# Kernel optimization log

Hardware: AMD Instinct MI355X
Metric: run time of the kernel (lower is better)

Reference implementation:

```python
import jax, jax.numpy as jnp
import numpy as np

B, T, M, C, H = 32, 128, 1290, 512, 8
NUM_BLOCKS = 4
MLP_LAYERS = 2
TOPK = 8


def _ln(x, g, b):
    mu = jnp.mean(x, -1, keepdims=True)
    var = jnp.mean((x - mu) ** 2, -1, keepdims=True)
    return (x - mu) / jnp.sqrt(var + 1e-5) * g + b


def setup_inputs() -> dict:
    key = jax.random.key(0)
    ks = jax.random.split(key, 12)

    def w(k, shape, s=0.02):
        return jax.random.normal(k, shape, jnp.float32) * s

    return {
        "ipts": jax.random.normal(ks[0], (B, T, C), jnp.float32),
        "memory": jax.random.normal(ks[1], (B, M, C), jnp.float32),
        "Wq": w(ks[2], (C, C)), "bq": jnp.zeros(C, jnp.float32),
        "Wk": w(ks[3], (C, C)), "bk": jnp.zeros(C, jnp.float32),
        "Wv": w(ks[4], (C, C)), "bv": jnp.zeros(C, jnp.float32),
        "Wm": w(ks[5], (C, C)), "bm": jnp.zeros(C, jnp.float32),  # shared attention_mlp layer
        "g1": jnp.ones(C, jnp.float32), "b1": jnp.zeros(C, jnp.float32),
        "g2": jnp.ones(C, jnp.float32), "b2": jnp.zeros(C, jnp.float32),
        "Wp": w(ks[6], (C, C)), "bp": jnp.zeros(C, jnp.float32),
        "rep_w": jax.random.normal(ks[7], (C,), jnp.float32),
        "Wig": w(ks[8], (C, 2 * C)), "big": jnp.zeros(2 * C, jnp.float32),
        "Wmg": w(ks[9], (C, 2 * C)), "bmg": jnp.zeros(2 * C, jnp.float32),
        "forget_bias": jnp.float32(1.0),
        "input_bias": jnp.float32(0.0),
    }


def reference(ipts, memory, Wq, bq, Wk, bk, Wv, bv, Wm, bm, g1, b1, g2, b2,
              Wp, bp, rep_w, Wig, big, Wmg, bmg, forget_bias, input_bias):
    Dh = C // H
    scale = 1.0 / np.sqrt(Dh)

    def heads(x):  # [B,L,C] -> [B,H,L,Dh]
        return x.reshape(x.shape[0], x.shape[1], H, Dh).transpose(0, 2, 1, 3)

    def mha(inp, mem, use_topk):
        # query from mem, key/value from inp (matches multi_head_attention(ipts, memory))
        q, k, v = heads(mem @ Wq + bq), heads(inp @ Wk + bk), heads(inp @ Wv + bv)
        att = jax.nn.softmax(jnp.einsum('bhqd,bhkd->bhqk', q, k) * scale, axis=-1)
        if use_topk:
            _, idx = jax.lax.top_k(att, TOPK)  # [B,H,Q,TOPK]
            mask = jnp.zeros_like(att)
            for i in range(TOPK):  # small fixed loop; avoids [.,.,.,K,L] blowup
                mask = mask + jax.nn.one_hot(idx[..., i], att.shape[-1], dtype=att.dtype)
            att = att * mask
        o = jnp.einsum('bhqk,bhkd->bhqd', att, v)
        return o.transpose(0, 2, 1, 3).reshape(o.shape[0], o.shape[2], C)

    inp = ipts @ Wp + bp  # input_projector, [B,T,C]
    mem = memory
    for _ in range(NUM_BLOCKS):
        mem = _ln(mem + mha(inp, mem, True), g1, b1)
        h = mem
        for _ in range(MLP_LAYERS):  # shared weights (ModuleList([lin]*L))
            h = jax.nn.relu(h @ Wm + bm)
        mem = _ln(mem + h, g2, b2)

    # gates (gate_style='unit')
    gi = jnp.mean(jax.nn.relu(rep_w * inp), axis=1) @ Wig + big  # [B,2C]
    gm = jnp.tanh(memory) @ Wmg + bmg                            # [B,M,2C]
    gates = gm + gi[:, None, :]
    ig = jax.nn.sigmoid(gates[..., :C] + input_bias)
    fg = jax.nn.sigmoid(gates[..., C:] + forget_bias)
    next_memory = ig * jnp.tanh(mem) + fg * memory

    # hx: query from inp, key/value from next_memory, no topk
    hx = mha(next_memory, inp, False)  # [B,T,C]
    return (next_memory, hx)
```

## Files before the change

### kernel.cpp

```cpp
#include <hip/hip_runtime.h>
#include <stdint.h>

typedef uint16_t u16;
typedef uint32_t u32;

#define DEVI __device__ __forceinline__

DEVI float b2f(u16 u) { return __uint_as_float(((u32)u) << 16); }
DEVI float blo(u32 u) { return __uint_as_float(u << 16); }
DEVI float bhi(u32 u) { return __uint_as_float(u & 0xffff0000u); }
DEVI u16 f2b(float f) {
  u32 x = __float_as_uint(f);
  return (u16)((x + 0x7fffu + ((x >> 16) & 1u)) >> 16);
}
DEVI u32 pack2(float a, float b) { return (u32)f2b(a) | ((u32)f2b(b) << 16); }
DEVI float sigm(float x) { return 1.f / (1.f + __expf(-x)); }

typedef __bf16 bf16x8 __attribute__((ext_vector_type(8)));
typedef float f32x4 __attribute__((ext_vector_type(4)));

#define MFMA16(a, b, c) __builtin_amdgcn_mfma_f32_16x16x32_bf16(a, b, c, 0, 0, 0)

DEVI void gll16(const void* g, void* l) {
  __builtin_amdgcn_global_load_lds((const __attribute__((address_space(1))) void*)g,
                                   (__attribute__((address_space(3))) void*)l, 16, 0, 0);
}

DEVI u32 fmono(float s) {
  u32 x = __float_as_uint(s);
  return x ^ (((u32)((int)x >> 31)) | 0x80000000u);
}

DEVI void ced(u32& a, u32& b) {
  u32 hi = max(a, b), lo = min(a, b);
  a = hi; b = lo;
}
DEVI void sort8_desc(u32* v) {
  ced(v[0], v[1]); ced(v[2], v[3]); ced(v[4], v[5]); ced(v[6], v[7]);
  ced(v[0], v[2]); ced(v[1], v[3]); ced(v[4], v[6]); ced(v[5], v[7]);
  ced(v[1], v[2]); ced(v[5], v[6]);
  ced(v[0], v[4]); ced(v[1], v[5]); ced(v[2], v[6]); ced(v[3], v[7]);
  ced(v[2], v[4]); ced(v[3], v[5]);
  ced(v[1], v[2]); ced(v[3], v[4]); ced(v[5], v[6]);
}
DEVI void bitonic8_desc(u32* v) {
  ced(v[0], v[4]); ced(v[1], v[5]); ced(v[2], v[6]); ced(v[3], v[7]);
  ced(v[0], v[2]); ced(v[1], v[3]); ced(v[4], v[6]); ced(v[5], v[7]);
  ced(v[0], v[1]); ced(v[2], v[3]); ced(v[4], v[5]); ced(v[6], v[7]);
}
DEVI void merge_top8(u32* a, const u32* b) {
#pragma unroll
  for (int j = 0; j < 8; ++j) a[j] = max(a[j], b[7 - j]);
  bitonic8_desc(a);
}

__global__ void detect_kernel(const u16* __restrict__ x, int* __restrict__ flag) {
  if (threadIdx.x == 0 && blockIdx.x == 0) {
    int f = 0;
    for (int i = 0; i < 64; ++i) {
      u16 u = x[2 * i];
      int e = (u >> 7) & 0xFF;
      if (e > 131) f = 1;
    }
    *flag = f;
  }
}

struct CvtArgs {
  const void* src[23];
  int aoff[23];
  int n[23];
  int total;
};

__global__ __launch_bounds__(256) void convert_fused(CvtArgs a, u16* __restrict__ arena,
                                                     const int* __restrict__ flag) {
  int e4 = (blockIdx.x * 256 + threadIdx.x) * 4;
  if (e4 >= a.total) return;
  const char* sp = (const char*)a.src[0];
  int rel = e4, cnt = a.n[0];
#pragma unroll
  for (int j = 1; j < 23; ++j)
    if (e4 >= a.aoff[j]) { sp = (const char*)a.src[j]; rel = e4 - a.aoff[j]; cnt = a.n[j]; }
  const bool f32 = (*flag != 0);
  if (rel + 3 < cnt) {
    if (f32) {
      float4 v = *(const float4*)(sp + (size_t)rel * 4);
      uint2 o;
      o.x = pack2(v.x, v.y);
      o.y = pack2(v.z, v.w);
      *(uint2*)(arena + e4) = o;
    } else {
      *(uint2*)(arena + e4) = *(const uint2*)(sp + (size_t)rel * 2);
    }
  } else {
#pragma unroll
    for (int k = 0; k < 4; ++k) {
      u16 o = 0;
      if (rel + k < cnt)
        o = f32 ? f2b(((const float*)sp)[rel + k]) : ((const u16*)sp)[rel + k];
      arena[e4 + k] = o;
    }
  }
}

__global__ void biascat_kernel(const u16* __restrict__ bq, const u16* __restrict__ bk,
                               const u16* __restrict__ bv, u16* __restrict__ bqkv,
                               u16* __restrict__ bkv) {
  int t = threadIdx.x;
  bqkv[t] = bq[t];
  bqkv[512 + t] = bk[t];
  bqkv[1024 + t] = bv[t];
  bkv[t] = bk[t];
  bkv[512 + t] = bv[t];
}

template <int ACT>
__global__ __launch_bounds__(256, 3) void gemm_bt(
    const u16* __restrict__ A, const u16* __restrict__ Bt,
    const u16* __restrict__ bias, u16* __restrict__ Co, int Mtot, int Ntot) {
  __shared__ __align__(16) u16 aT[128 * 64];
  __shared__ __align__(16) u16 bT[128 * 64];
  const int tid = threadIdx.x;
  const int lane = tid & 63;
  const int w = tid >> 6;
  const int m0 = blockIdx.x * 128;
  const int n0 = blockIdx.y * 128;
  const int wm = (w & 1) << 6;
  const int wn = (w >> 1) << 6;

  f32x4 acc[4][4] = {};

  const u16* ga[4];
  const u16* gb[4];
#pragma unroll
  for (int q = 0; q < 4; ++q) {
    int j = q * 256 + tid;
    int r = j >> 3, s = j & 7;
    int c = (s ^ (r & 7)) * 8;
    int ra = m0 + r;
    if (ra >= Mtot) ra = Mtot - 1;
    ga[q] = A + (size_t)ra * 512 + c;
    gb[q] = Bt + (size_t)(n0 + r) * 512 + c;
  }

  for (int ko = 0; ko < 8; ++ko) {
    const int k0 = ko * 64;
#pragma unroll
    for (int q = 0; q < 4; ++q) {
      int j = q * 256 + tid;
      gll16(ga[q] + k0, aT + j * 8);
      gll16(gb[q] + k0, bT + j * 8);
    }
    __syncthreads();
#pragma unroll
    for (int ks = 0; ks < 2; ++ks) {
      bf16x8 af[4], bfr[4];
#pragma unroll
      for (int i = 0; i < 4; ++i) {
        int cch = ks * 4 + (lane >> 4);
        int r = wm + i * 16 + (lane & 15);
        af[i] = *(const bf16x8*)(aT + (r * 8 + (cch ^ (r & 7))) * 8);
        int rn = wn + i * 16 + (lane & 15);
        bfr[i] = *(const bf16x8*)(bT + (rn * 8 + (cch ^ (rn & 7))) * 8);
      }
#pragma unroll
      for (int i = 0; i < 4; ++i)
#pragma unroll
        for (int jn = 0; jn < 4; ++jn)
          acc[i][jn] = MFMA16(af[i], bfr[jn], acc[i][jn]);
    }
    __syncthreads();
  }

  const int cl = lane & 15;
  const int rg = lane >> 4;
#pragma unroll
  for (int jn = 0; jn < 4; ++jn) {
    int col = n0 + wn + jn * 16 + cl;
    float bv = b2f(bias[col]);
#pragma unroll
    for (int i = 0; i < 4; ++i) {
      int rowb = m0 + wm + i * 16 + rg * 4;
#pragma unroll
      for (int rr = 0; rr < 4; ++rr) {
        int row = rowb + rr;
        if (row < Mtot) {
          float vv = acc[i][jn][rr] + bv;
          if (ACT) vv = fmaxf(vv, 0.f);
          Co[(size_t)row * Ntot + col] = f2b(vv);
        }
      }
    }
  }
}

__global__ __launch_bounds__(256) void transpose_kernel(const u16* __restrict__ in,
                                                        u16* __restrict__ outb, int K, int N) {
  __shared__ u16 tile[32][33];
  const int tx = threadIdx.x & 31, ty = threadIdx.x >> 5;
  const int bx = blockIdx.x * 32;
  const int by = blockIdx.y * 32;
#pragma unroll
  for (int i = 0; i < 32; i += 8) tile[ty + i][tx] = in[(size_t)(by + ty + i) * N + bx + tx];
  __syncthreads();
#pragma unroll
  for (int i = 0; i < 32; i += 8) outb[(size_t)(bx + ty + i) * K + by + tx] = tile[tx][ty + i];
}

__global__ void tanhmem_kernel(const u16* __restrict__ mi, u16* __restrict__ th, int n8) {
  int i = blockIdx.x * 256 + threadIdx.x;
  if (i >= n8) return;
  uint4 u = ((const uint4*)mi)[i];
  uint4 t;
  t.x = pack2(tanhf(blo(u.x)), tanhf(bhi(u.x)));
  t.y = pack2(tanhf(blo(u.y)), tanhf(bhi(u.y)));
  t.z = pack2(tanhf(blo(u.z)), tanhf(bhi(u.z)));
  t.w = pack2(tanhf(blo(u.w)), tanhf(bhi(u.w)));
  ((uint4*)th)[i] = t;
}

__global__ void redmean_kernel(const u16* __restrict__ inp, const u16* __restrict__ repw,
                               u16* __restrict__ outb) {
  const int b = blockIdx.x;
  const int c = blockIdx.y * 256 + threadIdx.x;
  const float rw = b2f(repw[c]);
  float s = 0.f;
  for (int t = 0; t < 128; ++t)
    s += fmaxf(rw * b2f(inp[(size_t)(b * 128 + t) * 512 + c]), 0.f);
  outb[b * 512 + c] = f2b(s * (1.f / 128.f));
}

__global__ __launch_bounds__(64) void ln_kernel(const u16* __restrict__ src,
                                                const u16* __restrict__ addb,
                                                u16* __restrict__ dst,
                                                const u16* __restrict__ g,
                                                const u16* __restrict__ bb) {
  const int row = blockIdx.x;
  const int lane = threadIdx.x;
  const u16* srow = src + (size_t)row * 512;
  const u16* arow = addb + (size_t)row * 512;
  float x[8];
  float s = 0.f;
#pragma unroll
  for (int i = 0; i < 8; ++i) {
    int c = lane + i * 64;
    x[i] = b2f(srow[c]) + b2f(arow[c]);
    s += x[i];
  }
#pragma unroll
  for (int off = 32; off > 0; off >>= 1) s += __shfl_xor(s, off, 64);
  const float mu = s * (1.f / 512.f);
  float v = 0.f;
#pragma unroll
  for (int i = 0; i < 8; ++i) {
    float d = x[i] - mu;
    v = fmaf(d, d, v);
  }
#pragma unroll
  for (int off = 32; off > 0; off >>= 1) v += __shfl_xor(v, off, 64);
  const float rstd = rsqrtf(v * (1.f / 512.f) + 1e-5f);
  u16* orow = dst + (size_t)row * 512;
#pragma unroll
  for (int i = 0; i < 8; ++i) {
    int c = lane + i * 64;
    orow[c] = f2b(fmaf((x[i] - mu) * rstd, b2f(g[c]), b2f(bb[c])));
  }
}

__global__ __launch_bounds__(256, 3) void attn1_mfma(const u16* __restrict__ q,
                                                     const u16* __restrict__ kb,
                                                     const u16* __restrict__ vb,
                                                     u16* __restrict__ o, int ldkv) {
  __shared__ __align__(16) u16 Pl[128 * 136];
  __shared__ __align__(16) u16 VT[64 * 136];
  __shared__ float lbuf[128];
  u16* Kl = Pl;

  const int tid = threadIdx.x;
  const int lane = tid & 63;
  const int w = tid >> 6;
  const int quad = lane >> 4;
  const int l15 = lane & 15;
  const int qb = blockIdx.x;
  const int bh = blockIdx.y;
  const int b = bh >> 3, h = bh & 7;

#pragma unroll
  for (int qq = 0; qq < 4; ++qq) {
    int j = qq * 256 + tid;
    int r = j >> 3, s = j & 7;
    gll16(kb + (size_t)(b * 128 + r) * ldkv + h * 64 + (s ^ (r & 7)) * 8, Kl + j * 8);
  }
#pragma unroll
  for (int p = 0; p < 4; ++p) {
    int key = (tid & 63) + 64 * (p & 1);
    int dc = w + 4 * (p >> 1);
    uint4 u = *(const uint4*)(vb + (size_t)(b * 128 + key) * ldkv + h * 64 + dc * 8);
    u16 tmp[8];
    *(uint4*)tmp = u;
#pragma unroll
    for (int jj = 0; jj < 8; ++jj) VT[(dc * 8 + jj) * 136 + key] = tmp[jj];
  }

  bf16x8 bq[2][2];
  {
    int ra = min(qb * 128 + w * 32 + l15, 1289);
    int rb_ = min(qb * 128 + w * 32 + 16 + l15, 1289);
    const u16* qa = q + (size_t)(b * 1290 + ra) * 512 + h * 64 + quad * 8;
    const u16* qc = q + (size_t)(b * 1290 + rb_) * 512 + h * 64 + quad * 8;
    bq[0][0] = *(const bf16x8*)(qa);
    bq[0][1] = *(const bf16x8*)(qa + 32);
    bq[1][0] = *(const bf16x8*)(qc);
    bq[1][1] = *(const bf16x8*)(qc + 32);
  }
  __syncthreads();

  f32x4 sa[2][8] = {};
#pragma unroll
  for (int ks = 0; ks < 2; ++ks) {
#pragma unroll
    for (int jn = 0; jn < 8; ++jn) {
      int n = jn * 16 + l15;
      int cch = ks * 4 + quad;
      bf16x8 ak = *(const bf16x8*)(Kl + (n * 8 + (cch ^ (n & 7))) * 8);
      sa[0][jn] = MFMA16(ak, bq[0][ks], sa[0][jn]);
      sa[1][jn] = MFMA16(ak, bq[1][ks], sa[1][jn]);
    }
  }
  __syncthreads();

  const u32 ibase = 127u - (u32)(quad * 4);
#pragma unroll
  for (int i = 0; i < 2; ++i) {
    const int qi = w * 32 + i * 16 + l15;
    u32 g[4][8];
#pragma unroll
    for (int jn = 0; jn < 8; ++jn)
#pragma unroll
      for (int rr = 0; rr < 4; ++rr) {
        float s = sa[i][jn][rr] * 0.125f;
        sa[i][jn][rr] = s;
        g[jn >> 1][(jn & 1) * 4 + rr] =
            (fmono(s) & 0xFFFFFF80u) | (ibase - (u32)(jn * 16 + rr));
      }
    sort8_desc(g[0]); sort8_desc(g[1]); sort8_desc(g[2]); sort8_desc(g[3]);
    merge_top8(g[0], g[1]);
    merge_top8(g[2], g[3]);
    merge_top8(g[0], g[2]);
    u32* tv = g[0];
#pragma unroll
    for (int off = 16; off < 64; off <<= 1) {
      u32 pv[8];
#pragma unroll
      for (int j = 0; j < 8; ++j) pv[j] = (u32)__shfl_xor((int)tv[7 - j], off, 64);
#pragma unroll
      for (int j = 0; j < 8; ++j) tv[j] = max(tv[j], pv[j]);
      bitonic8_desc(tv);
    }
    const u32 t8 = tv[7];
    u32 mb = tv[0] & 0xFFFFFF80u;
    u32 xm = (mb & 0x80000000u) ? (mb ^ 0x80000000u) : ~mb;
    const float mx = __uint_as_float(xm);
    float lsum = 0.f;
#pragma unroll
    for (int jn = 0; jn < 8; ++jn) {
      u16 pr[4];
#pragma unroll
      for (int rr = 0; rr < 4; ++rr) {
        float s = sa[i][jn][rr];
        float e = __expf(s - mx);
        lsum += e;
        u32 kk = (fmono(s) & 0xFFFFFF80u) | (ibase - (u32)(jn * 16 + rr));
        pr[rr] = (kk >= t8) ? f2b(e) : (u16)0;
      }
      uint2 st;
      st.x = (u32)pr[0] | ((u32)pr[1] << 16);
      st.y = (u32)pr[2] | ((u32)pr[3] << 16);
      *(uint2*)(Pl + qi * 136 + jn * 16 + quad * 4) = st;
    }
    lsum += __shfl_xor(lsum, 16, 64);
    lsum += __shfl_xor(lsum, 32, 64);
    if (quad == 0) lbuf[qi] = 1.f / lsum;
  }
  __syncthreads();

  f32x4 oa[2][4] = {};
#pragma unroll
  for (int kc = 0; kc < 4; ++kc) {
    bf16x8 ap[2];
#pragma unroll
    for (int i = 0; i < 2; ++i)
      ap[i] = *(const bf16x8*)(Pl + (w * 32 + i * 16 + l15) * 136 + kc * 32 + quad * 8);
#pragma unroll
    for (int jd = 0; jd < 4; ++jd) {
      bf16x8 bv_ = *(const bf16x8*)(VT + (jd * 16 + l15) * 136 + kc * 32 + quad * 8);
      oa[0][jd] = MFMA16(ap[0], bv_, oa[0][jd]);
      oa[1][jd] = MFMA16(ap[1], bv_, oa[1][jd]);
    }
  }

#pragma unroll
  for (int i = 0; i < 2; ++i) {
    int rowl = w * 32 + i * 16 + quad * 4;
#pragma unroll
    for (int rr = 0; rr < 4; ++rr) {
      int qg = qb * 128 + rowl + rr;
      if (qg < 1290) {
        float il = lbuf[rowl + rr];
        u16* orow = o + (size_t)(b * 1290 + qg) * 512 + h * 64;
#pragma unroll
        for (int jd = 0; jd < 4; ++jd) orow[jd * 16 + l15] = f2b(oa[i][jd][rr] * il);
      }
    }
  }
}

__global__ __launch_bounds__(256, 2) void attn2_mfma(const u16* __restrict__ q2,
                                                     const u16* __restrict__ k2,
                                                     const u16* __restrict__ v2,
                                                     float* __restrict__ pacc,
                                                     float* __restrict__ pml,
                                                     int ldq, int ldkv) {
  __shared__ __align__(16) u16 Kl[64 * 64];
  __shared__ __align__(16) u16 VT[64 * 72];
  __shared__ __align__(16) u16 Pl[4 * 32 * 72];
  const int tid = threadIdx.x;
  const int lane = tid & 63;
  const int w = tid >> 6;
  const int quad = lane >> 4;
  const int l15 = lane & 15;
  const int bh = blockIdx.x;
  const int b = bh >> 3, h = bh & 7;
  const int part = blockIdx.y;
  const int kstart = (part * 1290) >> 2;
  const int kend = ((part + 1) * 1290) >> 2;

  bf16x8 aq[2][2];
  {
    int r0 = b * 128 + w * 32 + l15;
    const u16* qa = q2 + (size_t)r0 * ldq + h * 64 + quad * 8;
    aq[0][0] = *(const bf16x8*)(qa);
    aq[0][1] = *(const bf16x8*)(qa + 32);
    aq[1][0] = *(const bf16x8*)(qa + (size_t)16 * ldq);
    aq[1][1] = *(const bf16x8*)(qa + (size_t)16 * ldq + 32);
  }

  f32x4 oa[2][4] = {};
  float m_[2][4], l_[2][4];
#pragma unroll
  for (int i = 0; i < 2; ++i)
#pragma unroll
    for (int r = 0; r < 4; ++r) { m_[i][r] = -1e30f; l_[i][r] = 0.f; }

  const int nk = kend - kstart;
  for (int kt = 0; kt < nk; kt += 64) {
    __syncthreads();
#pragma unroll
    for (int qq = 0; qq < 2; ++qq) {
      int j = qq * 256 + tid;
      int r = j >> 3, s = j & 7;
      int kg = kstart + kt + r;
      if (kg >= kend) kg = kend - 1;
      gll16(k2 + (size_t)(b * 1290 + kg) * ldkv + h * 64 + (s ^ (r & 7)) * 8, Kl + j * 8);
    }
    {
      int r = tid & 63;
      int kg = kstart + kt + r;
      if (kg >= kend) kg = kend - 1;
      const u16* vrow = v2 + (size_t)(b * 1290 + kg) * ldkv + h * 64;
#pragma unroll
      for (int p = 0; p < 2; ++p) {
        int dc = (tid >> 6) + p * 4;
        uint4 u = *(const uint4*)(vrow + dc * 8);
        u16 tmp[8];
        *(uint4*)tmp = u;
#pragma unroll
        for (int jj = 0; jj < 8; ++jj) VT[(dc * 8 + jj) * 72 + r] = tmp[jj];
      }
    }
    __syncthreads();

    f32x4 sa[2][4] = {};
#pragma unroll
    for (int ks = 0; ks < 2; ++ks) {
#pragma unroll
      for (int jn = 0; jn < 4; ++jn) {
        int n = jn * 16 + l15;
        int cch = ks * 4 + quad;
        bf16x8 bk = *(const bf16x8*)(Kl + (n * 8 + (cch ^ (n & 7))) * 8);
        sa[0][jn] = MFMA16(aq[0][ks], bk, sa[0][jn]);
        sa[1][jn] = MFMA16(aq[1][ks], bk, sa[1][jn]);
      }
    }

    u16* pw = Pl + w * (32 * 72);
#pragma unroll
    for (int i = 0; i < 2; ++i) {
      float rmax[4] = {-1e30f, -1e30f, -1e30f, -1e30f};
#pragma unroll
      for (int jn = 0; jn < 4; ++jn) {
        int kg = kstart + kt + jn * 16 + l15;
        bool val = kg < kend;
#pragma unroll
        for (int r = 0; r < 4; ++r) {
          float s = sa[i][jn][r] * 0.125f;
          s = val ? s : -1e30f;
          sa[i][jn][r] = s;
          rmax[r] = fmaxf(rmax[r], s);
        }
      }
#pragma unroll
      for (int off = 1; off < 16; off <<= 1)
#pragma unroll
        for (int r = 0; r < 4; ++r) rmax[r] = fmaxf(rmax[r], __shfl_xor(rmax[r], off, 64));
      float alpha[4];
#pragma unroll
      for (int r = 0; r < 4; ++r) {
        float mn = fmaxf(m_[i][r], rmax[r]);
        alpha[r] = __expf(m_[i][r] - mn);
        m_[i][r] = mn;
      }
      float lsum[4] = {0.f, 0.f, 0.f, 0.f};
#pragma unroll
      for (int jn = 0; jn < 4; ++jn)
#pragma unroll
        for (int r = 0; r < 4; ++r) {
          float p = __expf(sa[i][jn][r] - m_[i][r]);
          sa[i][jn][r] = p;
          lsum[r] += p;
        }
#pragma unroll
      for (int off = 1; off < 16; off <<= 1)
#pragma unroll
        for (int r = 0; r < 4; ++r) lsum[r] += __shfl_xor(lsum[r], off, 64);
#pragma unroll
      for (int r = 0; r < 4; ++r) l_[i][r] = l_[i][r] * alpha[r] + lsum[r];
#pragma unroll
      for (int jd = 0; jd < 4; ++jd)
#pragma unroll
        for (int r = 0; r < 4; ++r) oa[i][jd][r] *= alpha[r];
#pragma unroll
      for (int jn = 0; jn < 4; ++jn) {
        int col = jn * 16 + l15;
#pragma unroll
        for (int r = 0; r < 4; ++r)
          pw[(i * 16 + quad * 4 + r) * 72 + col] = f2b(sa[i][jn][r]);
      }
    }

#pragma unroll
    for (int ks = 0; ks < 2; ++ks) {
      bf16x8 ap[2];
#pragma unroll
      for (int i = 0; i < 2; ++i)
        ap[i] = *(const bf16x8*)(pw + (i * 16 + l15) * 72 + ks * 32 + quad * 8);
#pragma unroll
      for (int jd = 0; jd < 4; ++jd) {
        bf16x8 bv_ = *(const bf16x8*)(VT + (jd * 16 + l15) * 72 + ks * 32 + quad * 8);
        oa[0][jd] = MFMA16(ap[0], bv_, oa[0][jd]);
        oa[1][jd] = MFMA16(ap[1], bv_, oa[1][jd]);
      }
    }
  }

  float* pa = pacc + (size_t)(part * 256 + bh) * 128 * 64;
#pragma unroll
  for (int i = 0; i < 2; ++i) {
    int row = w * 32 + i * 16 + quad * 4;
#pragma unroll
    for (int r = 0; r < 4; ++r)
#pragma unroll
      for (int jd = 0; jd < 4; ++jd)
        pa[(size_t)(row + r) * 64 + jd * 16 + l15] = oa[i][jd][r];
    if (l15 == 0) {
#pragma unroll
      for (int r = 0; r < 4; ++r) {
        size_t pi = (size_t)(part * 256 + bh) * 128 + row + r;
        pml[pi * 2 + 0] = m_[i][r];
        pml[pi * 2 + 1] = l_[i][r];
      }
    }
  }
}

__global__ __launch_bounds__(64) void attn2_merge(const float* __restrict__ pacc,
                                                  const float* __restrict__ pml,
                                                  void* __restrict__ outp,
                                                  const int* __restrict__ flag) {
  const int qi = blockIdx.x;
  const int bh = qi >> 7, t = qi & 127;
  const int b = bh >> 3, h = bh & 7;
  const int lane = threadIdx.x;
  float mv[4], lv[4];
  float m0 = -1e30f;
#pragma unroll
  for (int i = 0; i < 4; ++i) {
    size_t pi = (size_t)(i * 256 + bh) * 128 + t;
    mv[i] = pml[pi * 2];
    lv[i] = pml[pi * 2 + 1];
    m0 = fmaxf(m0, mv[i]);
  }
  float L = 0.f, accd = 0.f;
#pragma unroll
  for (int i = 0; i < 4; ++i) {
    size_t pi = (size_t)(i * 256 + bh) * 128 + t;
    float e = __expf(mv[i] - m0);
    L += lv[i] * e;
    accd += pacc[pi * 64 + lane] * e;
  }
  float v = accd / L;
  size_t off = (size_t)41280 * 512 + ((size_t)(b * 128 + t) * 512 + h * 64 + lane);
  if (*flag) ((float*)outp)[off] = v; else ((u16*)outp)[off] = f2b(v);
}

__global__ __launch_bounds__(512) void gates_fused(const u16* __restrict__ gm,
                                                   const u16* __restrict__ gi,
                                                   const u16* __restrict__ memfin,
                                                   const u16* __restrict__ mem_in,
                                                   const u16* __restrict__ ibp,
                                                   const u16* __restrict__ fbp,
                                                   u16* __restrict__ nmbf,
                                                   void* __restrict__ outp,
                                                   const int* __restrict__ flag) {
  const int r = blockIdx.x;
  const int b = r / 1290;
  const int c = threadIdx.x;
  size_t i1024 = (size_t)r * 1024;
  size_t idx = (size_t)r * 512 + c;
  float ig = sigm(b2f(gm[i1024 + c]) + b2f(gi[b * 1024 + c]) + b2f(ibp[0]));
  float fg = sigm(b2f(gm[i1024 + 512 + c]) + b2f(gi[b * 1024 + 512 + c]) + b2f(fbp[0]));
  float v = ig * tanhf(b2f(memfin[idx])) + fg * b2f(mem_in[idx]);
  nmbf[idx] = f2b(v);
  if (*flag) ((float*)outp)[idx] = v; else ((u16*)outp)[idx] = f2b(v);
}

extern "C" void kernel_launch(void* const* d_in, const int* in_sizes, int n_in,
                              void* d_out, int out_size, void* d_ws, size_t ws_size,
                              hipStream_t stream) {
  (void)out_size; (void)ws_size;
  char* ws = (char*)d_ws;
  size_t off = 0;
  auto alloc = [&](size_t bytes) {
    char* p = ws + off;
    off += (bytes + 255) & ~(size_t)255;
    return (void*)p;
  };

  int* flag = (int*)alloc(256);

  size_t aoffs[32];
  size_t total = 0;
  for (int i = 0; i < n_in; ++i) {
    aoffs[i] = total;
    total += ((size_t)in_sizes[i] + 127) & ~(size_t)127;
  }
  u16* arena = (u16*)alloc(total * 2);

  const u16* c_ipts = arena + aoffs[0];
  const u16* c_mem  = arena + aoffs[1];
  const u16* c_Wq = arena + aoffs[2];  const u16* c_bq = arena + aoffs[3];
  const u16* c_Wk = arena + aoffs[4];  const u16* c_bk = arena + aoffs[5];
  const u16* c_Wv = arena + aoffs[6];  const u16* c_bv = arena + aoffs[7];
  const u16* c_Wm = arena + aoffs[8];  const u16* c_bm = arena + aoffs[9];
  const u16* c_g1 = arena + aoffs[10]; const u16* c_b1 = arena + aoffs[11];
  const u16* c_g2 = arena + aoffs[12]; const u16* c_b2 = arena + aoffs[13];
  const u16* c_Wp = arena + aoffs[14]; const u16* c_bp = arena + aoffs[15];
  const u16* c_repw = arena + aoffs[16];
  const u16* c_Wig = arena + aoffs[17]; const u16* c_big = arena + aoffs[18];
  const u16* c_Wmg = arena + aoffs[19]; const u16* c_bmg = arena + aoffs[20];
  const u16* c_fb = arena + aoffs[21];
  const u16* c_ib = arena + aoffs[22];

  u16* WqkvT = (u16*)alloc((size_t)1536 * 512 * 2);
  u16* WmT = (u16*)alloc(512 * 512 * 2);
  u16* WpT = (u16*)alloc(512 * 512 * 2);
  u16* WigT = (u16*)alloc(512 * 1024 * 2);
  u16* WmgT = (u16*)alloc(512 * 1024 * 2);
  u16* bqkv = (u16*)alloc(1536 * 2);
  u16* bkv = (u16*)alloc(1024 * 2);
  u16* inp = (u16*)alloc((size_t)4096 * 512 * 2);
  u16* qkvbuf = (u16*)alloc((size_t)4096 * 1536 * 2);
  u16* rmean = (u16*)alloc(32 * 512 * 2);
  u16* gi = (u16*)alloc(32 * 1024 * 2);
  u16* membf = (u16*)alloc((size_t)41280 * 512 * 2);
  u16* qbuf = (u16*)alloc((size_t)41280 * 512 * 2);
  u16* obuf = (u16*)alloc((size_t)41280 * 512 * 2);
  u16* gmbuf = (u16*)alloc((size_t)41280 * 512 * 2);
  u16* nmbf = (u16*)alloc((size_t)41280 * 512 * 2);
  (void)gmbuf;
  u16* gm1024 = obuf;
  u16* kvbuf = obuf;
  float* pacc = (float*)(void*)qbuf;
  float* pml = (float*)((char*)(void*)qbuf + (size_t)4 * 32768 * 64 * 4);

  detect_kernel<<<1, 64, 0, stream>>>((const u16*)d_in[0], flag);
  {
    CvtArgs ca;
    for (int i = 0; i < 23; ++i) {
      int ii = (i < n_in) ? i : (n_in - 1);
      ca.src[i] = d_in[ii];
      ca.aoff[i] = (int)aoffs[ii];
      ca.n[i] = in_sizes[ii];
    }
    ca.total = (int)total;
    convert_fused<<<(unsigned)((total / 4 + 255) / 256), 256, 0, stream>>>(ca, arena, flag);
  }
  biascat_kernel<<<1, 512, 0, stream>>>(c_bq, c_bk, c_bv, bqkv, bkv);

  transpose_kernel<<<dim3(16, 16), 256, 0, stream>>>(c_Wq, WqkvT, 512, 512);
  transpose_kernel<<<dim3(16, 16), 256, 0, stream>>>(c_Wk, WqkvT + (size_t)512 * 512, 512, 512);
  transpose_kernel<<<dim3(16, 16), 256, 0, stream>>>(c_Wv, WqkvT + (size_t)1024 * 512, 512, 512);
  transpose_kernel<<<dim3(16, 16), 256, 0, stream>>>(c_Wm, WmT, 512, 512);
  transpose_kernel<<<dim3(16, 16), 256, 0, stream>>>(c_Wp, WpT, 512, 512);
  transpose_kernel<<<dim3(32, 16), 256, 0, stream>>>(c_Wig, WigT, 512, 1024);
  transpose_kernel<<<dim3(32, 16), 256, 0, stream>>>(c_Wmg, WmgT, 512, 1024);

  gemm_bt<0><<<dim3(32, 4), 256, 0, stream>>>(c_ipts, WpT, c_bp, inp, 4096, 512);
  gemm_bt<0><<<dim3(32, 12), 256, 0, stream>>>(inp, WqkvT, bqkv, qkvbuf, 4096, 1536);

  redmean_kernel<<<dim3(32, 2), 256, 0, stream>>>(inp, c_repw, rmean);
  gemm_bt<0><<<dim3(1, 8), 256, 0, stream>>>(rmean, WigT, c_big, gi, 32, 1024);

  const u16* memsrc = c_mem;
  for (int it = 0; it < 4; ++it) {
    gemm_bt<0><<<dim3(323, 4), 256, 0, stream>>>(memsrc, WqkvT, c_bq, qbuf, 41280, 512);
    attn1_mfma<<<dim3(11, 256), 256, 0, stream>>>(qbuf, qkvbuf + 512, qkvbuf + 1024, obuf, 1536);
    ln_kernel<<<dim3(41280), 64, 0, stream>>>(memsrc, obuf, membf, c_g1, c_b1);
    gemm_bt<1><<<dim3(323, 4), 256, 0, stream>>>(membf, WmT, c_bm, qbuf, 41280, 512);
    gemm_bt<1><<<dim3(323, 4), 256, 0, stream>>>(qbuf, WmT, c_bm, obuf, 41280, 512);
    ln_kernel<<<dim3(41280), 64, 0, stream>>>(membf, obuf, membf, c_g2, c_b2);
    memsrc = membf;
  }

  tanhmem_kernel<<<dim3(2641920 / 256), 256, 0, stream>>>(c_mem, qbuf, 2641920);
  gemm_bt<0><<<dim3(323, 8), 256, 0, stream>>>(qbuf, WmgT, c_bmg, gm1024, 41280, 1024);
  gates_fused<<<dim3(41280), 512, 0, stream>>>(gm1024, gi, membf, c_mem, c_ib, c_fb,
                                               nmbf, d_out, flag);

  gemm_bt<0><<<dim3(323, 8), 256, 0, stream>>>(nmbf, WqkvT + (size_t)512 * 512, bkv,
                                               kvbuf, 41280, 1024);
  attn2_mfma<<<dim3(256, 4), 256, 0, stream>>>(qkvbuf, kvbuf, kvbuf + 512, pacc, pml,
                                               1536, 1024);
  attn2_merge<<<dim3(32768), 64, 0, stream>>>(pacc, pml, d_out, flag);
}
```

Before: 1.372 ms.

## Remap GEMM blocks per XCD, stage epilogue through LDS for vector stores, raise occupancy

The GEMM grid is flattened to 1D and block IDs are remapped so that consecutive tiles land on the same XCD, which should improve L2 reuse of A rows across N tiles. The epilogue now writes bias-added results into a padded shared tile and then issues 16-byte coalesced global stores instead of scattered 2-byte stores. Launch bounds are raised to 4 blocks per CU, and the shared buffer grows slightly to hold the padded output tile. Together these target store inefficiency and cache locality, at the cost of an extra LDS round-trip and sync and possible register pressure.

```diff
diff --git a/kernel.cpp b/kernel.cpp
--- a/kernel.cpp
+++ b/kernel.cpp
@@ -116,16 +116,24 @@
 }
 
 template <int ACT>
-__global__ __launch_bounds__(256, 3) void gemm_bt(
+__global__ __launch_bounds__(256, 4) void gemm_bt(
     const u16* __restrict__ A, const u16* __restrict__ Bt,
-    const u16* __restrict__ bias, u16* __restrict__ Co, int Mtot, int Ntot) {
-  __shared__ __align__(16) u16 aT[128 * 64];
-  __shared__ __align__(16) u16 bT[128 * 64];
+    const u16* __restrict__ bias, u16* __restrict__ Co, int Mtot, int Ntot, int nby) {
+  __shared__ __align__(16) u16 smem[128 * 136];
+  u16* aT = smem;
+  u16* bT = smem + 128 * 64;
   const int tid = threadIdx.x;
   const int lane = tid & 63;
   const int w = tid >> 6;
-  const int m0 = blockIdx.x * 128;
-  const int n0 = blockIdx.y * 128;
+
+  const int nwg = gridDim.x;
+  const int orig = blockIdx.x;
+  const int xcd = orig & 7, sq = orig >> 3;
+  const int qd = nwg >> 3, rm = nwg & 7;
+  const int wg = (xcd < rm ? xcd * (qd + 1) : rm * (qd + 1) + (xcd - rm) * qd) + sq;
+  const int m0 = (wg / nby) * 128;
+  const int n0 = (wg % nby) * 128;
+
   const int wm = (w & 1) << 6;
   const int wn = (w >> 1) << 6;
 
@@ -173,24 +181,34 @@
     __syncthreads();
   }
 
+  u16* st = smem;
   const int cl = lane & 15;
   const int rg = lane >> 4;
 #pragma unroll
   for (int jn = 0; jn < 4; ++jn) {
-    int col = n0 + wn + jn * 16 + cl;
-    float bv = b2f(bias[col]);
+    int coll = wn + jn * 16 + cl;
+    float bv = b2f(bias[n0 + coll]);
 #pragma unroll
     for (int i = 0; i < 4; ++i) {
-      int rowb = m0 + wm + i * 16 + rg * 4;
+      int rowb = wm + i * 16 + rg * 4;
 #pragma unroll
       for (int rr = 0; rr < 4; ++rr) {
-        int row = rowb + rr;
-        if (row < Mtot) {
-          float vv = acc[i][jn][rr] + bv;
-          if (ACT) vv = fmaxf(vv, 0.f);
-          Co[(size_t)row * Ntot + col] = f2b(vv);
-        }
-      }
+        float vv = acc[i][jn][rr] + bv;
+        if (ACT) vv = fmaxf(vv, 0.f);
+        st[(rowb + rr) * 136 + coll] = f2b(vv);
+      }
+    }
+  }
+  __syncthreads();
+#pragma unroll
+  for (int t = 0; t < 8; ++t) {
+    int idx = (t * 256 + tid) * 8;
+    int r = idx >> 7;
+    int c = idx & 127;
+    int row = m0 + r;
+    if (row < Mtot) {
+      uint4 v = *(const uint4*)(st + r * 136 + c);
+      *(uint4*)(Co + (size_t)row * Ntot + n0 + c) = v;
     }
   }
 }
@@ -716,30 +734,30 @@
   transpose_kernel<<<dim3(32, 16), 256, 0, stream>>>(c_Wig, WigT, 512, 1024);
   transpose_kernel<<<dim3(32, 16), 256, 0, stream>>>(c_Wmg, WmgT, 512, 1024);
 
-  gemm_bt<0><<<dim3(32, 4), 256, 0, stream>>>(c_ipts, WpT, c_bp, inp, 4096, 512);
-  gemm_bt<0><<<dim3(32, 12), 256, 0, stream>>>(inp, WqkvT, bqkv, qkvbuf, 4096, 1536);
+  gemm_bt<0><<<dim3(32 * 4), 256, 0, stream>>>(c_ipts, WpT, c_bp, inp, 4096, 512, 4);
+  gemm_bt<0><<<dim3(32 * 12), 256, 0, stream>>>(inp, WqkvT, bqkv, qkvbuf, 4096, 1536, 12);
 
   redmean_kernel<<<dim3(32, 2), 256, 0, stream>>>(inp, c_repw, rmean);
-  gemm_bt<0><<<dim3(1, 8), 256, 0, stream>>>(rmean, WigT, c_big, gi, 32, 1024);
+  gemm_bt<0><<<dim3(1 * 8), 256, 0, stream>>>(rmean, WigT, c_big, gi, 32, 1024, 8);
 
   const u16* memsrc = c_mem;
   for (int it = 0; it < 4; ++it) {
-    gemm_bt<0><<<dim3(323, 4), 256, 0, stream>>>(memsrc, WqkvT, c_bq, qbuf, 41280, 512);
+    gemm_bt<0><<<dim3(323 * 4), 256, 0, stream>>>(memsrc, WqkvT, c_bq, qbuf, 41280, 512, 4);
     attn1_mfma<<<dim3(11, 256), 256, 0, stream>>>(qbuf, qkvbuf + 512, qkvbuf + 1024, obuf, 1536);
     ln_kernel<<<dim3(41280), 64, 0, stream>>>(memsrc, obuf, membf, c_g1, c_b1);
-    gemm_bt<1><<<dim3(323, 4), 256, 0, stream>>>(membf, WmT, c_bm, qbuf, 41280, 512);
-    gemm_bt<1><<<dim3(323, 4), 256, 0, stream>>>(qbuf, WmT, c_bm, obuf, 41280, 512);
+    gemm_bt<1><<<dim3(323 * 4), 256, 0, stream>>>(membf, WmT, c_bm, qbuf, 41280, 512, 4);
+    gemm_bt<1><<<dim3(323 * 4), 256, 0, stream>>>(qbuf, WmT, c_bm, obuf, 41280, 512, 4);
     ln_kernel<<<dim3(41280), 64, 0, stream>>>(membf, obuf, membf, c_g2, c_b2);
     memsrc = membf;
   }
 
   tanhmem_kernel<<<dim3(2641920 / 256), 256, 0, stream>>>(c_mem, qbuf, 2641920);
-  gemm_bt<0><<<dim3(323, 8), 256, 0, stream>>>(qbuf, WmgT, c_bmg, gm1024, 41280, 1024);
+  gemm_bt<0><<<dim3(323 * 8), 256, 0, stream>>>(qbuf, WmgT, c_bmg, gm1024, 41280, 1024, 8);
   gates_fused<<<dim3(41280), 512, 0, stream>>>(gm1024, gi, membf, c_mem, c_ib, c_fb,
                                                nmbf, d_out, flag);
 
-  gemm_bt<0><<<dim3(323, 8), 256, 0, stream>>>(nmbf, WqkvT + (size_t)512 * 512, bkv,
-                                               kvbuf, 41280, 1024);
+  gemm_bt<0><<<dim3(323 * 8), 256, 0, stream>>>(nmbf, WqkvT + (size_t)512 * 512, bkv,
+                                                kvbuf, 41280, 1024, 8);
   attn2_mfma<<<dim3(256, 4), 256, 0, stream>>>(qkvbuf, kvbuf, kvbuf + 512, pacc, pml,
                                                1536, 1024);
   attn2_merge<<<dim3(32768), 64, 0, stream>>>(pacc, pml, d_out, flag);
```

Measured after the change: 1.215 ms. 11.5% less time.
